# Kernel optimization log

Measured on AMD Instinct MI355X. Metric: run time of the kernel, lower is better.

Reference implementation:

```python
import jax, jax.numpy as jnp
import numpy as np
from jax import lax

B, T, D = 2, 2048, 2048
H, DK, DV = 16, 128, 128
K = 4  # conv kernel size
KEY_DIM = H * DK      # 2048
VAL_DIM = H * DV      # 2048
CONV_DIM = 2 * KEY_DIM + VAL_DIM  # 6144
EPS = 1e-6


def setup_inputs() -> dict:
    key = jax.random.key(0)
    ks = jax.random.split(key, 10)
    s = lambda fan: 1.0 / np.sqrt(fan)
    return {
        "hidden_states": jax.random.normal(ks[0], (B, T, D), jnp.float32),
        "W_qkv": jax.random.normal(ks[1], (D, CONV_DIM), jnp.float32) * s(D),
        "conv_w": jax.random.normal(ks[2], (CONV_DIM, 1, K), jnp.float32) * s(K),
        "W_z": jax.random.normal(ks[3], (D, VAL_DIM), jnp.float32) * s(D),
        "W_b": jax.random.normal(ks[4], (D, H), jnp.float32) * s(D),
        "W_a": jax.random.normal(ks[5], (D, H), jnp.float32) * s(D),
        "dt_bias": jnp.ones((H,), jnp.float32),
        "A_log": jnp.log(jax.random.uniform(ks[6], (H,), jnp.float32, 1e-3, 16.0)),
        "norm_weight": jnp.ones((DV,), jnp.float32),
        "W_out": jax.random.normal(ks[7], (VAL_DIM, D), jnp.float32) * s(VAL_DIM),
    }


def _l2norm(x):
    return x * lax.rsqrt(jnp.sum(x * x, axis=-1, keepdims=True) + 1e-6)


def _gated_delta_rule(q, k, v, g, beta):
    """q,k: [B,T,H,DK]; v: [B,T,H,DV]; g,beta: [B,T,H]. Returns o: [B,T,H,DV]."""
    # time-major for scan
    qT, kT, vT = (jnp.moveaxis(x, 1, 0) for x in (q, k, v))  # [T,B,H,d]
    gT = jnp.moveaxis(g, 1, 0)      # [T,B,H]
    bT = jnp.moveaxis(beta, 1, 0)   # [T,B,H]

    def step(S, inp):
        q_t, k_t, v_t, g_t, b_t = inp
        S = S * jnp.exp(g_t)[..., None, None]                      # decay [B,H,DK,DV]
        kv_mem = jnp.einsum("bhk,bhkv->bhv", k_t, S)               # S^T k
        delta = (v_t - kv_mem) * b_t[..., None]                     # beta-scaled error
        S = S + jnp.einsum("bhk,bhv->bhkv", k_t, delta)
        o_t = jnp.einsum("bhk,bhkv->bhv", q_t, S)
        return S, o_t

    S0 = jnp.zeros((q.shape[0], H, DK, DV), q.dtype)
    _, oT = lax.scan(step, S0, (qT, kT, vT, gT, bT))
    return jnp.moveaxis(oT, 0, 1)  # [B,T,H,DV]


def reference(hidden_states, W_qkv, conv_w, W_z, W_b, W_a, dt_bias, A_log,
              norm_weight, W_out):
    Bs, Ts, _ = hidden_states.shape

    # qkv projection + depthwise causal conv1d + silu
    mixed = hidden_states @ W_qkv                      # [B,T,CONV_DIM]
    xc = jnp.moveaxis(mixed, 1, 2)                     # [B,C,T]
    xc = lax.conv_general_dilated(xc, conv_w, (1,), [(K - 1, 0)],
                                  feature_group_count=CONV_DIM)
    mixed = jax.nn.silu(jnp.moveaxis(xc, 1, 2))        # [B,T,C]

    q, k, v = jnp.split(mixed, [KEY_DIM, 2 * KEY_DIM], axis=-1)
    q = _l2norm(q.reshape(Bs, Ts, H, DK)) * (DK ** -0.5)
    k = _l2norm(k.reshape(Bs, Ts, H, DK))
    v = v.reshape(Bs, Ts, H, DV)

    beta = jax.nn.sigmoid(hidden_states @ W_b)                     # [B,T,H]
    g = -jnp.exp(A_log) * jax.nn.softplus(hidden_states @ W_a + dt_bias)

    o = _gated_delta_rule(q, k, v, g, beta)            # [B,T,H,DV]

    # gated RMSNorm (Mamba2-style: gate first, then normalize)
    z = (hidden_states @ W_z).reshape(Bs, Ts, H, DV)
    o = o * jax.nn.silu(z)
    var = jnp.mean(o * o, axis=-1, keepdims=True)
    o = o * lax.rsqrt(var + EPS) * norm_weight

    return o.reshape(Bs, Ts, VAL_DIM) @ W_out          # [B,T,D]
```

## Files before the change

### kernel.cpp

```cpp
#include <hip/hip_runtime.h>

#define B_ 2
#define T_ 2048
#define D_ 2048
#define H_ 16
#define CONV_DIM_ 6144
#define NC_ 32
#define CK_ 64

typedef __bf16 bf16;
typedef bf16 bf16x8 __attribute__((ext_vector_type(8)));
typedef bf16 bf16x4 __attribute__((ext_vector_type(4)));
typedef float floatx4 __attribute__((ext_vector_type(4)));

__device__ __forceinline__ void async_copy16(bf16* lds, const bf16* g) {
    auto* g1 = (const __attribute__((address_space(1))) unsigned int*)g;
    auto* l3 = (__attribute__((address_space(3))) unsigned int*)lds;
    __builtin_amdgcn_global_load_lds(g1, l3, 16, 0, 0);
}

__global__ void cvt_bf16_kernel(const float* __restrict__ in, bf16* __restrict__ out, int n4) {
    int i = blockIdx.x * 256 + threadIdx.x;
    if (i < n4) {
        float4 v = ((const float4*)in)[i];
        bf16x4 o = { (bf16)v.x, (bf16)v.y, (bf16)v.z, (bf16)v.w };
        *(bf16x4*)(out + 4 * (size_t)i) = o;
    }
}

__global__ void transpose_kernel(const float* __restrict__ in, bf16* __restrict__ out, int R, int Cn) {
    __shared__ float tile[32][33];
    const int c0 = blockIdx.x << 5, r0 = blockIdx.y << 5;
    const int tx = threadIdx.x & 31, ty = threadIdx.x >> 5;
#pragma unroll
    for (int i = 0; i < 4; ++i) {
        int r = ty + (i << 3);
        tile[r][tx] = in[(size_t)(r0 + r) * Cn + c0 + tx];
    }
    __syncthreads();
#pragma unroll
    for (int i = 0; i < 4; ++i) {
        int cc = ty + (i << 3);
        out[(size_t)(c0 + cc) * R + r0 + tx] = (bf16)tile[tx][cc];
    }
}

__global__ void wba_cvt_kernel(const float* __restrict__ Wb, const float* __restrict__ Wa,
                               bf16* __restrict__ Wba) {
    int idx = blockIdx.x * 256 + threadIdx.x;
    int d = idx >> 4, h = idx & 15;
    Wba[(size_t)h * 2048 + d]        = (bf16)Wb[idx];
    Wba[(size_t)(h + 16) * 2048 + d] = (bf16)Wa[idx];
}

template <typename OutT>
__global__ __launch_bounds__(256) void gemm_kernel(
    const bf16* __restrict__ A, const bf16* __restrict__ Bt, OutT* __restrict__ C,
    int M, int N, int K) {
    __shared__ bf16 As[128 * 64];
    __shared__ bf16 Bs[128 * 64];
    const int tid = threadIdx.x;
    const int m0 = blockIdx.y << 7;
    const int n0 = blockIdx.x << 7;
    const int wave = tid >> 6, lane = tid & 63;
    const int wm = (wave >> 1) << 6, wn = (wave & 1) << 6;
    const int lrow = lane & 15, quad = lane >> 4;
    const int rl = lane >> 3;
    const int c8s = (lane & 7) ^ (rl & 7);

    floatx4 acc[4][4];
#pragma unroll
    for (int mt = 0; mt < 4; ++mt)
#pragma unroll
        for (int nt = 0; nt < 4; ++nt)
            acc[mt][nt] = floatx4{0.f, 0.f, 0.f, 0.f};

    for (int k0 = 0; k0 < K; k0 += 64) {
        __syncthreads();
#pragma unroll
        for (int i = 0; i < 4; ++i) {
            const int slot = wave * 4 + i;
            const int r = slot * 8 + rl;
            async_copy16(&As[slot * 512], A + (size_t)(m0 + r) * K + k0 + c8s * 8);
            async_copy16(&Bs[slot * 512], Bt + (size_t)(n0 + r) * K + k0 + c8s * 8);
        }
        __syncthreads();
#pragma unroll
        for (int kk = 0; kk < 64; kk += 32) {
            const int sw = (((kk >> 3) + quad) ^ (lrow & 7)) << 3;
            bf16x8 af[4], bfr[4];
#pragma unroll
            for (int mt = 0; mt < 4; ++mt) {
                af[mt]  = *(const bf16x8*)(&As[((wm + (mt << 4) + lrow) << 6) + sw]);
                bfr[mt] = *(const bf16x8*)(&Bs[((wn + (mt << 4) + lrow) << 6) + sw]);
            }
#pragma unroll
            for (int mt = 0; mt < 4; ++mt)
#pragma unroll
                for (int nt = 0; nt < 4; ++nt)
                    acc[mt][nt] = __builtin_amdgcn_mfma_f32_16x16x32_bf16(af[mt], bfr[nt], acc[mt][nt], 0, 0, 0);
        }
    }
#pragma unroll
    for (int mt = 0; mt < 4; ++mt)
#pragma unroll
        for (int nt = 0; nt < 4; ++nt) {
            const int col = n0 + wn + (nt << 4) + lrow;
            const int rowb = m0 + wm + (mt << 4) + (quad << 2);
#pragma unroll
            for (int i2 = 0; i2 < 4; ++i2)
                C[(size_t)(rowb + i2) * N + col] = (OutT)acc[mt][nt][i2];
        }
}

__global__ __launch_bounds__(512, 2) void gemm256_kernel(
    const bf16* __restrict__ A, const bf16* __restrict__ Bt,
    bf16* __restrict__ C0, bf16* __restrict__ C1,
    int M, int Ncat, int K, int split, int ld0, int ld1) {
    __shared__ bf16 As[4][256 * 32];
    __shared__ bf16 Bs[4][256 * 32];
    const int tid = threadIdx.x;
    const int wave = tid >> 6, lane = tid & 63;
    const int quad = lane >> 4, lrow = lane & 15;
    const int wm = (wave >> 2) << 7;
    const int wn = (wave & 3) << 6;
    const int m0 = blockIdx.y << 8, n0 = blockIdx.x << 8;

    const bf16* gA[2];
    const bf16* gB[2];
#pragma unroll
    for (int i = 0; i < 2; ++i) {
        const int q = wave * 2 + i;
        const int u = (lane & 7) ^ (lane >> 3);
        const int row = (q * 8 + (lane >> 3)) * 2 + (u >> 2);
        const int col = (u & 3) * 8;
        gA[i] = A  + (size_t)(m0 + row) * K + col;
        gB[i] = Bt + (size_t)(n0 + row) * K + col;
    }

    auto loff = [](int row, int qd) -> int {
        return ((row >> 1) << 6) + (((((row & 1) << 2) | qd) ^ ((row >> 1) & 7)) << 3);
    };

    floatx4 acc[8][4];
#pragma unroll
    for (int mt = 0; mt < 8; ++mt)
#pragma unroll
        for (int nt = 0; nt < 4; ++nt)
            acc[mt][nt] = floatx4{0.f, 0.f, 0.f, 0.f};

    const int KT = K >> 5;

#pragma unroll
    for (int t = 0; t < 3; ++t) {
        async_copy16(&As[t][(wave * 2 + 0) * 512], gA[0] + t * 32);
        async_copy16(&As[t][(wave * 2 + 1) * 512], gA[1] + t * 32);
        async_copy16(&Bs[t][(wave * 2 + 0) * 512], gB[0] + t * 32);
        async_copy16(&Bs[t][(wave * 2 + 1) * 512], gB[1] + t * 32);
    }
    asm volatile("s_waitcnt vmcnt(8)" ::: "memory");
    __builtin_amdgcn_s_barrier();

    for (int t = 0; t < KT; ++t) {
        const int b = t & 3;
        const bf16* as = &As[b][0];
        const bf16* bs = &Bs[b][0];
        bf16x8 bfr[4], af[4];
#pragma unroll
        for (int nt = 0; nt < 4; ++nt)
            bfr[nt] = *(const bf16x8*)(bs + loff(wn + nt * 16 + lrow, quad));
#pragma unroll
        for (int mt = 0; mt < 4; ++mt)
            af[mt] = *(const bf16x8*)(as + loff(wm + mt * 16 + lrow, quad));
        if (t + 2 < KT)       asm volatile("s_waitcnt vmcnt(4)" ::: "memory");
        else if (t + 2 == KT) asm volatile("s_waitcnt vmcnt(0)" ::: "memory");
        if (t + 3 < KT) {
            const int bn = (t + 3) & 3;
            async_copy16(&As[bn][(wave * 2 + 0) * 512], gA[0] + (t + 3) * 32);
            async_copy16(&As[bn][(wave * 2 + 1) * 512], gA[1] + (t + 3) * 32);
        }
        __builtin_amdgcn_s_barrier();
        asm volatile("s_waitcnt lgkmcnt(0)" ::: "memory");
        __builtin_amdgcn_sched_barrier(0);
        __builtin_amdgcn_s_setprio(1);
#pragma unroll
        for (int mt = 0; mt < 4; ++mt)
#pragma unroll
            for (int nt = 0; nt < 4; ++nt)
                acc[mt][nt] = __builtin_amdgcn_mfma_f32_16x16x32_bf16(
                    af[mt], bfr[nt], acc[mt][nt], 0, 0, 0);
        __builtin_amdgcn_s_setprio(0);
        __builtin_amdgcn_sched_barrier(0);
        __builtin_amdgcn_s_barrier();
#pragma unroll
        for (int mt = 0; mt < 4; ++mt)
            af[mt] = *(const bf16x8*)(as + loff(wm + 64 + mt * 16 + lrow, quad));
        if (t + 3 < KT) {
            const int bn = (t + 3) & 3;
            async_copy16(&Bs[bn][(wave * 2 + 0) * 512], gB[0] + (t + 3) * 32);
            async_copy16(&Bs[bn][(wave * 2 + 1) * 512], gB[1] + (t + 3) * 32);
        }
        __builtin_amdgcn_s_barrier();
        asm volatile("s_waitcnt lgkmcnt(0)" ::: "memory");
        __builtin_amdgcn_sched_barrier(0);
        __builtin_amdgcn_s_setprio(1);
#pragma unroll
        for (int mt = 0; mt < 4; ++mt)
#pragma unroll
            for (int nt = 0; nt < 4; ++nt)
                acc[4 + mt][nt] = __builtin_amdgcn_mfma_f32_16x16x32_bf16(
                    af[mt], bfr[nt], acc[4 + mt][nt], 0, 0, 0);
        __builtin_amdgcn_s_setprio(0);
        __builtin_amdgcn_sched_barrier(0);
        __builtin_amdgcn_s_barrier();
    }

    const bool second = (n0 >= split);
    bf16* Cp = second ? C1 : C0;
    const int ldc = second ? ld1 : ld0;
    const int nc0 = second ? n0 - split : n0;
#pragma unroll
    for (int mt = 0; mt < 8; ++mt)
#pragma unroll
        for (int nt = 0; nt < 4; ++nt) {
            const int col = nc0 + wn + nt * 16 + lrow;
            const int rowb = m0 + wm + mt * 16 + (quad << 2);
#pragma unroll
            for (int i2 = 0; i2 < 4; ++i2)
                Cp[(size_t)(rowb + i2) * ldc + col] = (bf16)acc[mt][nt][i2];
        }
}

__global__ __launch_bounds__(256) void conv_silu_kernel(
    const bf16* __restrict__ mixed, const float* __restrict__ cw,
    bf16* __restrict__ qb, bf16* __restrict__ kb, bf16* __restrict__ vb) {
    const int bt = blockIdx.y;
    const int t = bt & (T_ - 1);
    const int b = bt >> 11;
    const int c0 = blockIdx.x * 2048 + threadIdx.x * 8;
    const size_t base = (size_t)bt * CONV_DIM_ + c0;

    bf16x8 zz;
#pragma unroll
    for (int j = 0; j < 8; ++j) zz[j] = (bf16)0.f;
    const bf16x8 r3 = *(const bf16x8*)(mixed + base);
    const bf16x8 r2 = (t >= 1) ? *(const bf16x8*)(mixed + base - CONV_DIM_) : zz;
    const bf16x8 r1 = (t >= 2) ? *(const bf16x8*)(mixed + base - 2 * CONV_DIM_) : zz;
    const bf16x8 r0 = (t >= 3) ? *(const bf16x8*)(mixed + base - 3 * CONV_DIM_) : zz;

    const float4* cw4 = (const float4*)cw;
    float vals[8];
    float ss = 0.f;
#pragma unroll
    for (int j = 0; j < 8; ++j) {
        const float4 w = cw4[c0 + j];
        float acc = (float)r3[j] * w.w + (float)r2[j] * w.z +
                    (float)r1[j] * w.y + (float)r0[j] * w.x;
        const float sv = acc / (1.f + __expf(-acc));
        vals[j] = sv;
        ss += sv * sv;
    }

    if (c0 < 4096) {
#pragma unroll
        for (int o = 1; o < 16; o <<= 1) ss += __shfl_xor(ss, o);
        const float scale = rsqrtf(ss + 1e-6f);
        const bool isq = c0 < 2048;
        const float mul = isq ? scale * 0.08838834764831845f : scale;
        const int h = (c0 >> 7) & 15;
        const int d0 = c0 & 127;
        const size_t oidx = (((size_t)(b * H_ + h)) * T_ + t) * 128 + d0;
        bf16x8 o8;
#pragma unroll
        for (int j = 0; j < 8; ++j) o8[j] = (bf16)(vals[j] * mul);
        *(bf16x8*)((isq ? qb : kb) + oidx) = o8;
    } else {
        const int h = (c0 >> 7) & 15;
        const int d0 = c0 & 127;
        const size_t oidx = (((size_t)(b * H_ + h)) * T_ + t) * 128 + d0;
        bf16x8 o8;
#pragma unroll
        for (int j = 0; j < 8; ++j) o8[j] = (bf16)vals[j];
        *(bf16x8*)(vb + oidx) = o8;
    }
}

__global__ __launch_bounds__(256) void gbeta_mfma_kernel(
    const bf16* __restrict__ Xb, const bf16* __restrict__ Wba,
    const float* __restrict__ dtb, const float* __restrict__ Alog,
    float* __restrict__ gbuf, float* __restrict__ bbuf) {
    const int tid = threadIdx.x, wave = tid >> 6, lane = tid & 63;
    const int ln = lane & 15, qd = lane >> 4;
    const int m0 = blockIdx.x * 64 + wave * 16;
    floatx4 acc0 = {0.f, 0.f, 0.f, 0.f}, acc1 = {0.f, 0.f, 0.f, 0.f};
    const bf16* arow = Xb + (size_t)(m0 + ln) * 2048 + qd * 8;
    const bf16* b0 = Wba + (size_t)ln * 2048 + qd * 8;
    const bf16* b1 = Wba + (size_t)(16 + ln) * 2048 + qd * 8;
    for (int k = 0; k < 2048; k += 32) {
        bf16x8 af  = *(const bf16x8*)(arow + k);
        bf16x8 bf0 = *(const bf16x8*)(b0 + k);
        bf16x8 bf1 = *(const bf16x8*)(b1 + k);
        acc0 = __builtin_amdgcn_mfma_f32_16x16x32_bf16(af, bf0, acc0, 0, 0, 0);
        acc1 = __builtin_amdgcn_mfma_f32_16x16x32_bf16(af, bf1, acc1, 0, 0, 0);
    }
    const float dtbv = dtb[ln], al = __expf(Alog[ln]);
#pragma unroll
    for (int ii = 0; ii < 4; ++ii) {
        const int row = m0 + qd * 4 + ii;
        const int t = row & (T_ - 1), b = row >> 11;
        const size_t o = ((size_t)(b * H_ + ln)) * T_ + t;
        bbuf[o] = 1.f / (1.f + __expf(-acc0[ii]));
        const float xx = acc1[ii] + dtbv;
        const float sp = (xx > 15.f) ? xx : log1pf(__expf(xx));
        gbuf[o] = -al * sp;
    }
}

__global__ __launch_bounds__(256) void qkkt_kernel(const bf16* __restrict__ qb, const bf16* __restrict__ kb,
                                                   float* __restrict__ Araw, float* __restrict__ Mraw) {
    const int u = blockIdx.x;
    const int bh = u >> 5, nc = u & 31;
    const int t0 = nc * CK_;
    const int tid = threadIdx.x, wave = tid >> 6, lane = tid & 63;
    const int qd = lane >> 4, ln = lane & 15;
    __shared__ bf16 Kc[64 * 136], Qc[64 * 136];
    const size_t kbase = ((size_t)bh * T_ + t0) * 128;
#pragma unroll
    for (int it = 0; it < 4; ++it) {
        int idx = it * 256 + tid;
        int row = idx >> 4, c8 = idx & 15;
        *(uint4*)(&Kc[row * 136 + c8 * 8]) = *(const uint4*)(kb + kbase + row * 128 + c8 * 8);
        *(uint4*)(&Qc[row * 136 + c8 * 8]) = *(const uint4*)(qb + kbase + row * 128 + c8 * 8);
    }
    __syncthreads();
#pragma unroll
    for (int nt = 0; nt < 4; ++nt) {
        floatx4 accA = {0.f, 0.f, 0.f, 0.f}, accM = {0.f, 0.f, 0.f, 0.f};
#pragma unroll
        for (int kk = 0; kk < 4; ++kk) {
            bf16x8 bfr = *(const bf16x8*)(&Kc[(nt * 16 + ln) * 136 + kk * 32 + qd * 8]);
            bf16x8 afK = *(const bf16x8*)(&Kc[(wave * 16 + ln) * 136 + kk * 32 + qd * 8]);
            bf16x8 afQ = *(const bf16x8*)(&Qc[(wave * 16 + ln) * 136 + kk * 32 + qd * 8]);
            accA = __builtin_amdgcn_mfma_f32_16x16x32_bf16(afK, bfr, accA, 0, 0, 0);
            accM = __builtin_amdgcn_mfma_f32_16x16x32_bf16(afQ, bfr, accM, 0, 0, 0);
        }
#pragma unroll
        for (int ii = 0; ii < 4; ++ii) {
            int i = wave * 16 + qd * 4 + ii, j = nt * 16 + ln;
            Araw[(size_t)u * 4096 + i * 64 + j] = accA[ii];
            Mraw[(size_t)u * 4096 + i * 64 + j] = accM[ii];
        }
    }
}

__global__ __launch_bounds__(64) void prep_kernel(
    const float* __restrict__ gbuf, const float* __restrict__ bbuf,
    const float* __restrict__ Araw, const float* __restrict__ Mraw,
    float* __restrict__ lamg, float* __restrict__ ratiog,
    bf16* __restrict__ Tg, bf16* __restrict__ Mg) {
    const int u = blockIdx.x, bh = u >> 5, nc = u & 31, t0 = nc * CK_;
    const int lane = threadIdx.x;
    __shared__ float L[64 * 65];
    __shared__ float cv[64], bv[64];
    float g = gbuf[(size_t)bh * T_ + t0 + lane];
    float beta = bbuf[(size_t)bh * T_ + t0 + lane];
    float c = g;
#pragma unroll
    for (int off = 1; off < 64; off <<= 1) {
        float tval = __shfl_up(c, off);
        if (lane >= off) c += tval;
    }
    float c63 = __shfl(c, 63);
    lamg[(size_t)u * 64 + lane] = __expf(c);
    ratiog[(size_t)u * 64 + lane] = __expf(c63 - c);
    cv[lane] = c; bv[lane] = beta;
    __syncthreads();
    for (int i = 0; i < 64; ++i) {
        float a = Araw[(size_t)u * 4096 + i * 64 + lane];
        L[i * 65 + lane] = (lane < i) ? bv[i] * __expf(cv[i] - c) * a : 0.f;
    }
    __syncthreads();
    float t[64];
#pragma unroll
    for (int i = 0; i < 64; ++i) t[i] = (i == lane) ? 1.f : 0.f;
#pragma unroll
    for (int j = 0; j < 63; ++j) {
#pragma unroll
        for (int i = j + 1; i < 64; ++i)
            t[i] -= L[i * 65 + j] * t[j];
    }
#pragma unroll
    for (int i = 0; i < 64; ++i)
        Tg[(size_t)u * 4096 + i * 64 + lane] = (bf16)t[i];
    for (int i = 0; i < 64; ++i) {
        float m = Mraw[(size_t)u * 4096 + i * 64 + lane];
        float mij = (lane <= i) ? __expf(cv[i] - c) * m : 0.f;
        Mg[(size_t)u * 4096 + i * 64 + lane] = (bf16)mij;
    }
}

struct Pref {
    uint4 t2[2], m2[2];
    bf16x8 kf[4], qf[4];
    bf16x8 ktf[2][2];
    float rrv[4], vv[4], lam[4], bet[4], lamlast;
};

__device__ __forceinline__ void load_pref(
    Pref& p, int u, int t0, size_t kbase, int tid, int wave, int ln, int qd,
    int bh, int vbase,
    const bf16* __restrict__ qb, const bf16* __restrict__ kb, const bf16* __restrict__ vb,
    const bf16* __restrict__ Tg, const bf16* __restrict__ Mg,
    const float* __restrict__ lamg, const float* __restrict__ ratiog,
    const float* __restrict__ bbuf) {
#pragma unroll
    for (int it = 0; it < 2; ++it) {
        int idx = it * 256 + tid;
        int row = idx >> 3, c8 = idx & 7;
        p.t2[it] = *(const uint4*)(Tg + (size_t)u * 4096 + row * 64 + c8 * 8);
        p.m2[it] = *(const uint4*)(Mg + (size_t)u * 4096 + row * 64 + c8 * 8);
    }
    const size_t rowoff = kbase + (size_t)(wave * 16 + ln) * 128;
#pragma unroll
    for (int kk = 0; kk < 4; ++kk) {
        p.kf[kk] = *(const bf16x8*)(kb + rowoff + kk * 32 + qd * 8);
        p.qf[kk] = *(const bf16x8*)(qb + rowoff + kk * 32 + qd * 8);
    }
    const int i0 = wave * 16 + qd * 4;
#pragma unroll
    for (int ii = 0; ii < 4; ++ii) {
        p.vv[ii]  = (float)vb[kbase + (size_t)(i0 + ii) * 128 + vbase + ln];
        p.lam[ii] = lamg[(size_t)u * 64 + i0 + ii];
        p.bet[ii] = bbuf[(size_t)bh * T_ + t0 + i0 + ii];
        p.rrv[ii] = ratiog[(size_t)u * 64 + i0 + ii];
    }
    p.lamlast = lamg[(size_t)u * 64 + 63];
#pragma unroll
    for (int mt = 0; mt < 2; ++mt) {
        const int kd = (wave * 2 + mt) * 16 + ln;
#pragma unroll
        for (int kk2 = 0; kk2 < 2; ++kk2) {
            const int ib = kk2 * 32 + qd * 8;
#pragma unroll
            for (int j = 0; j < 8; ++j)
                p.ktf[mt][kk2][j] = kb[kbase + (size_t)(ib + j) * 128 + kd];
        }
    }
}

__global__ __launch_bounds__(256) void seq_kernel(
    const bf16* __restrict__ qb, const bf16* __restrict__ kb, const bf16* __restrict__ vb,
    const bf16* __restrict__ Tg, const bf16* __restrict__ Mg,
    const float* __restrict__ lamg, const float* __restrict__ ratiog,
    const float* __restrict__ bbuf, float* __restrict__ ob) {
    const int bh = blockIdx.x & 31;
    const int vs = blockIdx.x >> 5;
    const int vbase = vs * 16;
    const int tid = threadIdx.x;
    const int wave = tid >> 6, lane = tid & 63;
    const int qd = lane >> 4, ln = lane & 15;

    __shared__ bf16 Tt[64 * 72], Mm[64 * 72];
    __shared__ bf16 bT[16 * 72], Dt[16 * 72], Dtr[16 * 72];
    __shared__ bf16 Sbf[2][16 * 136];

    for (int idx = tid; idx < 2 * 16 * 136; idx += 256)
        (&Sbf[0][0])[idx] = (bf16)0.f;

    floatx4 Sreg[2] = { floatx4{0.f, 0.f, 0.f, 0.f}, floatx4{0.f, 0.f, 0.f, 0.f} };

    auto chunk_body = [&](Pref& cur, Pref& nxt, int nc, bf16* Srd, bf16* Swr) {
        const int t0 = nc * CK_;
        const size_t kbase = ((size_t)bh * T_ + t0) * 128;

#pragma unroll
        for (int it = 0; it < 2; ++it) {
            int idx = it * 256 + tid;
            int row = idx >> 3, c8 = idx & 7;
            *(uint4*)(&Tt[row * 72 + c8 * 8]) = cur.t2[it];
            *(uint4*)(&Mm[row * 72 + c8 * 8]) = cur.m2[it];
        }

        {
            const int ncn = (nc + 1 < NC_) ? nc + 1 : nc;
            load_pref(nxt, bh * NC_ + ncn, ncn * CK_, ((size_t)bh * T_ + (size_t)ncn * CK_) * 128,
                      tid, wave, ln, qd, bh, vbase, qb, kb, vb, Tg, Mg, lamg, ratiog, bbuf);
        }

        floatx4 ks = {0.f, 0.f, 0.f, 0.f};
#pragma unroll
        for (int kk = 0; kk < 4; ++kk) {
            bf16x8 bf = *(const bf16x8*)(&Srd[ln * 136 + kk * 32 + qd * 8]);
            ks = __builtin_amdgcn_mfma_f32_16x16x32_bf16(cur.kf[kk], bf, ks, 0, 0, 0);
        }
        {
            const int i0 = wave * 16 + qd * 4;
            bf16x4 bw;
#pragma unroll
            for (int ii = 0; ii < 4; ++ii)
                bw[ii] = (bf16)(cur.bet[ii] * (cur.vv[ii] - cur.lam[ii] * ks[ii]));
            *(bf16x4*)(&bT[ln * 72 + i0]) = bw;
        }
        __syncthreads();

        {
            floatx4 acc = {0.f, 0.f, 0.f, 0.f};
#pragma unroll
            for (int kk = 0; kk < 2; ++kk) {
                bf16x8 af = *(const bf16x8*)(&Tt[(wave * 16 + ln) * 72 + kk * 32 + qd * 8]);
                bf16x8 bf = *(const bf16x8*)(&bT[ln * 72 + kk * 32 + qd * 8]);
                acc = __builtin_amdgcn_mfma_f32_16x16x32_bf16(af, bf, acc, 0, 0, 0);
            }
            const int i0 = wave * 16 + qd * 4;
            bf16x4 dw = { (bf16)acc[0], (bf16)acc[1], (bf16)acc[2], (bf16)acc[3] };
            *(bf16x4*)(&Dt[ln * 72 + i0]) = dw;
            bf16x4 dwr = { (bf16)(acc[0] * cur.rrv[0]), (bf16)(acc[1] * cur.rrv[1]),
                           (bf16)(acc[2] * cur.rrv[2]), (bf16)(acc[3] * cur.rrv[3]) };
            *(bf16x4*)(&Dtr[ln * 72 + i0]) = dwr;
        }
        __syncthreads();

        {
            floatx4 acc = {0.f, 0.f, 0.f, 0.f};
#pragma unroll
            for (int kk = 0; kk < 4; ++kk) {
                bf16x8 bf = *(const bf16x8*)(&Srd[ln * 136 + kk * 32 + qd * 8]);
                acc = __builtin_amdgcn_mfma_f32_16x16x32_bf16(cur.qf[kk], bf, acc, 0, 0, 0);
            }
            floatx4 o;
#pragma unroll
            for (int ii = 0; ii < 4; ++ii) o[ii] = acc[ii] * cur.lam[ii];
#pragma unroll
            for (int kk = 0; kk < 2; ++kk) {
                bf16x8 af = *(const bf16x8*)(&Mm[(wave * 16 + ln) * 72 + kk * 32 + qd * 8]);
                bf16x8 bf = *(const bf16x8*)(&Dt[ln * 72 + kk * 32 + qd * 8]);
                o = __builtin_amdgcn_mfma_f32_16x16x32_bf16(af, bf, o, 0, 0, 0);
            }
            const int i0 = wave * 16 + qd * 4;
#pragma unroll
            for (int ii = 0; ii < 4; ++ii)
                ob[kbase + (size_t)(i0 + ii) * 128 + vbase + ln] = o[ii];
        }
#pragma unroll
        for (int mt = 0; mt < 2; ++mt) {
            const int kt = wave * 2 + mt;
            floatx4 acc = {0.f, 0.f, 0.f, 0.f};
#pragma unroll
            for (int kk = 0; kk < 2; ++kk) {
                bf16x8 bf = *(const bf16x8*)(&Dtr[ln * 72 + kk * 32 + qd * 8]);
                acc = __builtin_amdgcn_mfma_f32_16x16x32_bf16(cur.ktf[mt][kk], bf, acc, 0, 0, 0);
            }
            floatx4 sold = Sreg[mt];
#pragma unroll
            for (int ii = 0; ii < 4; ++ii) sold[ii] = sold[ii] * cur.lamlast + acc[ii];
            Sreg[mt] = sold;
            bf16x4 sb4 = { (bf16)sold[0], (bf16)sold[1], (bf16)sold[2], (bf16)sold[3] };
            *(bf16x4*)(&Swr[ln * 136 + kt * 16 + qd * 4]) = sb4;
        }
        __syncthreads();
    };

    Pref pA, pB;
    load_pref(pA, bh * NC_, 0, (size_t)bh * T_ * 128, tid, wave, ln, qd, bh, vbase,
              qb, kb, vb, Tg, Mg, lamg, ratiog, bbuf);
    __syncthreads();

#pragma unroll 1
    for (int nc2 = 0; nc2 < NC_; nc2 += 2) {
        chunk_body(pA, pB, nc2,     &Sbf[0][0], &Sbf[1][0]);
        chunk_body(pB, pA, nc2 + 1, &Sbf[1][0], &Sbf[0][0]);
    }
}

__global__ void gated_norm_kernel(const float* __restrict__ ob, const bf16* __restrict__ z,
                                  const float* __restrict__ nw, bf16* __restrict__ onorm) {
    const int idx = blockIdx.x;
    const int h = idx & (H_ - 1);
    const int bt = idx >> 4;
    const int t = bt & (T_ - 1);
    const int b = bt >> 11;
    const int tid = threadIdx.x;
    const size_t obase = (((size_t)(b * H_ + h)) * T_ + t) * 128;
    const size_t zbase = (size_t)bt * 2048 + (h << 7);
    float o1 = ob[obase + tid], o2 = ob[obase + tid + 64];
    const float z1 = (float)z[zbase + tid], z2 = (float)z[zbase + tid + 64];
    o1 *= z1 / (1.f + __expf(-z1));
    o2 *= z2 / (1.f + __expf(-z2));
    float ss = o1 * o1 + o2 * o2;
#pragma unroll
    for (int o = 1; o < 64; o <<= 1) ss += __shfl_xor(ss, o);
    const float scale = rsqrtf(ss * (1.f / 128.f) + 1e-6f);
    onorm[zbase + tid]      = (bf16)(o1 * scale * nw[tid]);
    onorm[zbase + tid + 64] = (bf16)(o2 * scale * nw[tid + 64]);
}

extern "C" void kernel_launch(void* const* d_in, const int* in_sizes, int n_in,
                              void* d_out, int out_size, void* d_ws, size_t ws_size,
                              hipStream_t stream) {
    const float* X    = (const float*)d_in[0];
    const float* Wqkv = (const float*)d_in[1];
    const float* cw   = (const float*)d_in[2];
    const float* Wz   = (const float*)d_in[3];
    const float* Wb   = (const float*)d_in[4];
    const float* Wa   = (const float*)d_in[5];
    const float* dtb  = (const float*)d_in[6];
    const float* Alog = (const float*)d_in[7];
    const float* nw   = (const float*)d_in[8];
    const float* Wout = (const float*)d_in[9];
    float* out = (float*)d_out;

    char* ws = (char*)d_ws;
    size_t off = 0;
    auto alloc = [&](size_t bytes) -> char* {
        char* p = ws + off;
        off += (bytes + 255) & ~(size_t)255;
        return p;
    };
    bf16*  Xb      = (bf16*)alloc((size_t)B_ * T_ * D_ * 2);
    char*  wcat_p  = alloc((size_t)8192 * 2048 * 2);
    bf16*  Wcat    = (bf16*)wcat_p;
    bf16*  Woutt   = (bf16*)alloc((size_t)D_ * D_ * 2);
    bf16*  Wba     = (bf16*)alloc((size_t)32 * 2048 * 2);
    char*  mixed_p = alloc((size_t)B_ * T_ * CONV_DIM_ * 2);
    bf16*  mixedb  = (bf16*)mixed_p;
    bf16*  zb      = (bf16*)alloc((size_t)B_ * T_ * D_ * 2);
    bf16*  kbuf    = (bf16*)alloc((size_t)B_ * T_ * D_ * 2);
    bf16*  vbuf    = (bf16*)alloc((size_t)B_ * T_ * D_ * 2);
    float* gbuf    = (float*)alloc((size_t)B_ * T_ * H_ * 4);
    float* bbuf    = (float*)alloc((size_t)B_ * T_ * H_ * 4);
    float* Mraw    = (float*)alloc((size_t)1024 * 4096 * 4);
    bf16*  Tg      = (bf16*)alloc((size_t)1024 * 4096 * 2);
    bf16*  Mg      = (bf16*)alloc((size_t)1024 * 4096 * 2);
    float* lamg    = (float*)alloc((size_t)1024 * 64 * 4);
    float* ratiog  = (float*)alloc((size_t)1024 * 64 * 4);
    bf16*  qbuf    = (bf16*)wcat_p;
    float* obuf    = (float*)mixed_p;
    float* Araw    = (float*)(mixed_p + (size_t)B_ * T_ * D_ * 4);
    bf16*  onorm   = (bf16*)Xb;

    cvt_bf16_kernel<<<dim3((B_ * T_ * D_ / 4 + 255) / 256), dim3(256), 0, stream>>>(X, Xb, B_ * T_ * D_ / 4);
    transpose_kernel<<<dim3(CONV_DIM_ / 32, D_ / 32), dim3(256), 0, stream>>>(Wqkv, Wcat, D_, CONV_DIM_);
    transpose_kernel<<<dim3(D_ / 32, D_ / 32), dim3(256), 0, stream>>>(Wz, Wcat + (size_t)CONV_DIM_ * D_, D_, D_);
    transpose_kernel<<<dim3(D_ / 32, D_ / 32), dim3(256), 0, stream>>>(Wout, Woutt, D_, D_);
    wba_cvt_kernel<<<dim3(128), dim3(256), 0, stream>>>(Wb, Wa, Wba);

    gemm256_kernel<<<dim3(8192 / 256, B_ * T_ / 256), dim3(512), 0, stream>>>(
        Xb, Wcat, mixedb, zb, B_ * T_, 8192, D_, CONV_DIM_, CONV_DIM_, D_);

    gbeta_mfma_kernel<<<dim3(64), dim3(256), 0, stream>>>(Xb, Wba, dtb, Alog, gbuf, bbuf);
    conv_silu_kernel<<<dim3(CONV_DIM_ / 2048, B_ * T_), dim3(256), 0, stream>>>(mixedb, cw, qbuf, kbuf, vbuf);

    qkkt_kernel<<<dim3(1024), dim3(256), 0, stream>>>(qbuf, kbuf, Araw, Mraw);
    prep_kernel<<<dim3(1024), dim3(64), 0, stream>>>(gbuf, bbuf, Araw, Mraw, lamg, ratiog, Tg, Mg);
    seq_kernel<<<dim3(256), dim3(256), 0, stream>>>(qbuf, kbuf, vbuf, Tg, Mg, lamg, ratiog, bbuf, obuf);

    gated_norm_kernel<<<dim3(B_ * T_ * H_), dim3(64), 0, stream>>>(obuf, zb, nw, onorm);

    gemm_kernel<float><<<dim3(D_ / 128, B_ * T_ / 128), dim3(256), 0, stream>>>(
        onorm, Woutt, out, B_ * T_, D_, D_);
}
```

Measured before the change: 602.4 us.

## Fuse QK^T and chunk prep kernels, split sequential scan into narrower value slices

Merges qkkt_kernel and prep_kernel into one kernel. The Gram matrices now stay in LDS instead of making an fp32 round trip through global memory. Inside that kernel, wave 0 runs the triangular solve while the other waves build the masked decay matrix. The sequential scan now covers 8 value columns per block instead of 16, doubling the grid to 512 blocks for more parallelism. In exchange, half of every MFMA tile in the scan is padding, so the compute per block stays the same while the total MFMA work doubles.

```diff
diff --git a/kernel.cpp b/kernel.cpp
--- a/kernel.cpp
+++ b/kernel.cpp
@@ -316,14 +316,19 @@
     }
 }
 
-__global__ __launch_bounds__(256) void qkkt_kernel(const bf16* __restrict__ qb, const bf16* __restrict__ kb,
-                                                   float* __restrict__ Araw, float* __restrict__ Mraw) {
+__global__ __launch_bounds__(256) void qkkt_prep_kernel(
+    const bf16* __restrict__ qb, const bf16* __restrict__ kb,
+    const float* __restrict__ gbuf, const float* __restrict__ bbuf,
+    float* __restrict__ lamg, float* __restrict__ ratiog,
+    bf16* __restrict__ Tg, bf16* __restrict__ Mg) {
     const int u = blockIdx.x;
     const int bh = u >> 5, nc = u & 31;
     const int t0 = nc * CK_;
     const int tid = threadIdx.x, wave = tid >> 6, lane = tid & 63;
     const int qd = lane >> 4, ln = lane & 15;
     __shared__ bf16 Kc[64 * 136], Qc[64 * 136];
+    __shared__ float Af[64 * 65], Mf[64 * 65];
+    __shared__ float cv[64], bv[64];
     const size_t kbase = ((size_t)bh * T_ + t0) * 128;
 #pragma unroll
     for (int it = 0; it < 4; ++it) {
@@ -332,7 +337,22 @@
         *(uint4*)(&Kc[row * 136 + c8 * 8]) = *(const uint4*)(kb + kbase + row * 128 + c8 * 8);
         *(uint4*)(&Qc[row * 136 + c8 * 8]) = *(const uint4*)(qb + kbase + row * 128 + c8 * 8);
     }
+    if (wave == 0) {
+        float g = gbuf[(size_t)bh * T_ + t0 + lane];
+        float beta = bbuf[(size_t)bh * T_ + t0 + lane];
+        float c = g;
+#pragma unroll
+        for (int off = 1; off < 64; off <<= 1) {
+            float tval = __shfl_up(c, off);
+            if (lane >= off) c += tval;
+        }
+        float c63 = __shfl(c, 63);
+        lamg[(size_t)u * 64 + lane] = __expf(c);
+        ratiog[(size_t)u * 64 + lane] = __expf(c63 - c);
+        cv[lane] = c; bv[lane] = beta;
+    }
     __syncthreads();
+    floatx4 rA[4], rM[4];
 #pragma unroll
     for (int nt = 0; nt < 4; ++nt) {
         floatx4 accA = {0.f, 0.f, 0.f, 0.f}, accM = {0.f, 0.f, 0.f, 0.f};
@@ -344,58 +364,43 @@
             accA = __builtin_amdgcn_mfma_f32_16x16x32_bf16(afK, bfr, accA, 0, 0, 0);
             accM = __builtin_amdgcn_mfma_f32_16x16x32_bf16(afQ, bfr, accM, 0, 0, 0);
         }
+        rA[nt] = accA; rM[nt] = accM;
+    }
+#pragma unroll
+    for (int nt = 0; nt < 4; ++nt)
 #pragma unroll
         for (int ii = 0; ii < 4; ++ii) {
             int i = wave * 16 + qd * 4 + ii, j = nt * 16 + ln;
-            Araw[(size_t)u * 4096 + i * 64 + j] = accA[ii];
-            Mraw[(size_t)u * 4096 + i * 64 + j] = accM[ii];
-        }
-    }
-}
-
-__global__ __launch_bounds__(64) void prep_kernel(
-    const float* __restrict__ gbuf, const float* __restrict__ bbuf,
-    const float* __restrict__ Araw, const float* __restrict__ Mraw,
-    float* __restrict__ lamg, float* __restrict__ ratiog,
-    bf16* __restrict__ Tg, bf16* __restrict__ Mg) {
-    const int u = blockIdx.x, bh = u >> 5, nc = u & 31, t0 = nc * CK_;
-    const int lane = threadIdx.x;
-    __shared__ float L[64 * 65];
-    __shared__ float cv[64], bv[64];
-    float g = gbuf[(size_t)bh * T_ + t0 + lane];
-    float beta = bbuf[(size_t)bh * T_ + t0 + lane];
-    float c = g;
-#pragma unroll
-    for (int off = 1; off < 64; off <<= 1) {
-        float tval = __shfl_up(c, off);
-        if (lane >= off) c += tval;
-    }
-    float c63 = __shfl(c, 63);
-    lamg[(size_t)u * 64 + lane] = __expf(c);
-    ratiog[(size_t)u * 64 + lane] = __expf(c63 - c);
-    cv[lane] = c; bv[lane] = beta;
+            Af[i * 65 + j] = rA[nt][ii];
+            Mf[i * 65 + j] = rM[nt][ii];
+        }
     __syncthreads();
-    for (int i = 0; i < 64; ++i) {
-        float a = Araw[(size_t)u * 4096 + i * 64 + lane];
-        L[i * 65 + lane] = (lane < i) ? bv[i] * __expf(cv[i] - c) * a : 0.f;
+#pragma unroll
+    for (int r = 0; r < 16; ++r) {
+        const int i = wave * 16 + r;
+        float a = Af[i * 65 + lane];
+        Af[i * 65 + lane] = (lane < i) ? bv[i] * __expf(cv[i] - cv[lane]) * a : 0.f;
     }
     __syncthreads();
-    float t[64];
-#pragma unroll
-    for (int i = 0; i < 64; ++i) t[i] = (i == lane) ? 1.f : 0.f;
-#pragma unroll
-    for (int j = 0; j < 63; ++j) {
-#pragma unroll
-        for (int i = j + 1; i < 64; ++i)
-            t[i] -= L[i * 65 + j] * t[j];
-    }
-#pragma unroll
-    for (int i = 0; i < 64; ++i)
-        Tg[(size_t)u * 4096 + i * 64 + lane] = (bf16)t[i];
-    for (int i = 0; i < 64; ++i) {
-        float m = Mraw[(size_t)u * 4096 + i * 64 + lane];
-        float mij = (lane <= i) ? __expf(cv[i] - c) * m : 0.f;
-        Mg[(size_t)u * 4096 + i * 64 + lane] = (bf16)mij;
+    if (wave == 0) {
+        float t[64];
+#pragma unroll
+        for (int i = 0; i < 64; ++i) t[i] = (i == lane) ? 1.f : 0.f;
+#pragma unroll
+        for (int j = 0; j < 63; ++j) {
+#pragma unroll
+            for (int i = j + 1; i < 64; ++i)
+                t[i] -= Af[i * 65 + j] * t[j];
+        }
+#pragma unroll
+        for (int i = 0; i < 64; ++i)
+            Tg[(size_t)u * 4096 + i * 64 + lane] = (bf16)t[i];
+    } else {
+        for (int i = wave - 1; i < 64; i += 3) {
+            float m = Mf[i * 65 + lane];
+            float mij = (lane <= i) ? __expf(cv[i] - cv[lane]) * m : 0.f;
+            Mg[(size_t)u * 4096 + i * 64 + lane] = (bf16)mij;
+        }
     }
 }
 
@@ -429,7 +434,7 @@
     const int i0 = wave * 16 + qd * 4;
 #pragma unroll
     for (int ii = 0; ii < 4; ++ii) {
-        p.vv[ii]  = (float)vb[kbase + (size_t)(i0 + ii) * 128 + vbase + ln];
+        p.vv[ii]  = (ln < 8) ? (float)vb[kbase + (size_t)(i0 + ii) * 128 + vbase + ln] : 0.f;
         p.lam[ii] = lamg[(size_t)u * 64 + i0 + ii];
         p.bet[ii] = bbuf[(size_t)bh * T_ + t0 + i0 + ii];
         p.rrv[ii] = ratiog[(size_t)u * 64 + i0 + ii];
@@ -455,7 +460,7 @@
     const float* __restrict__ bbuf, float* __restrict__ ob) {
     const int bh = blockIdx.x & 31;
     const int vs = blockIdx.x >> 5;
-    const int vbase = vs * 16;
+    const int vbase = vs * 8;
     const int tid = threadIdx.x;
     const int wave = tid >> 6, lane = tid & 63;
     const int qd = lane >> 4, ln = lane & 15;
@@ -466,6 +471,9 @@
 
     for (int idx = tid; idx < 2 * 16 * 136; idx += 256)
         (&Sbf[0][0])[idx] = (bf16)0.f;
+    for (int idx = tid; idx < 16 * 72; idx += 256) {
+        bT[idx] = (bf16)0.f; Dt[idx] = (bf16)0.f; Dtr[idx] = (bf16)0.f;
+    }
 
     floatx4 Sreg[2] = { floatx4{0.f, 0.f, 0.f, 0.f}, floatx4{0.f, 0.f, 0.f, 0.f} };
 
@@ -537,9 +545,11 @@
                 o = __builtin_amdgcn_mfma_f32_16x16x32_bf16(af, bf, o, 0, 0, 0);
             }
             const int i0 = wave * 16 + qd * 4;
-#pragma unroll
-            for (int ii = 0; ii < 4; ++ii)
-                ob[kbase + (size_t)(i0 + ii) * 128 + vbase + ln] = o[ii];
+            if (ln < 8) {
+#pragma unroll
+                for (int ii = 0; ii < 4; ++ii)
+                    ob[kbase + (size_t)(i0 + ii) * 128 + vbase + ln] = o[ii];
+            }
         }
 #pragma unroll
         for (int mt = 0; mt < 2; ++mt) {
@@ -628,14 +638,12 @@
     bf16*  vbuf    = (bf16*)alloc((size_t)B_ * T_ * D_ * 2);
     float* gbuf    = (float*)alloc((size_t)B_ * T_ * H_ * 4);
     float* bbuf    = (float*)alloc((size_t)B_ * T_ * H_ * 4);
-    float* Mraw    = (float*)alloc((size_t)1024 * 4096 * 4);
     bf16*  Tg      = (bf16*)alloc((size_t)1024 * 4096 * 2);
     bf16*  Mg      = (bf16*)alloc((size_t)1024 * 4096 * 2);
     float* lamg    = (float*)alloc((size_t)1024 * 64 * 4);
     float* ratiog  = (float*)alloc((size_t)1024 * 64 * 4);
     bf16*  qbuf    = (bf16*)wcat_p;
     float* obuf    = (float*)mixed_p;
-    float* Araw    = (float*)(mixed_p + (size_t)B_ * T_ * D_ * 4);
     bf16*  onorm   = (bf16*)Xb;
 
     cvt_bf16_kernel<<<dim3((B_ * T_ * D_ / 4 + 255) / 256), dim3(256), 0, stream>>>(X, Xb, B_ * T_ * D_ / 4);
@@ -650,9 +658,8 @@
     gbeta_mfma_kernel<<<dim3(64), dim3(256), 0, stream>>>(Xb, Wba, dtb, Alog, gbuf, bbuf);
     conv_silu_kernel<<<dim3(CONV_DIM_ / 2048, B_ * T_), dim3(256), 0, stream>>>(mixedb, cw, qbuf, kbuf, vbuf);
 
-    qkkt_kernel<<<dim3(1024), dim3(256), 0, stream>>>(qbuf, kbuf, Araw, Mraw);
-    prep_kernel<<<dim3(1024), dim3(64), 0, stream>>>(gbuf, bbuf, Araw, Mraw, lamg, ratiog, Tg, Mg);
-    seq_kernel<<<dim3(256), dim3(256), 0, stream>>>(qbuf, kbuf, vbuf, Tg, Mg, lamg, ratiog, bbuf, obuf);
+    qkkt_prep_kernel<<<dim3(1024), dim3(256), 0, stream>>>(qbuf, kbuf, gbuf, bbuf, lamg, ratiog, Tg, Mg);
+    seq_kernel<<<dim3(512), dim3(256), 0, stream>>>(qbuf, kbuf, vbuf, Tg, Mg, lamg, ratiog, bbuf, obuf);
 
     gated_norm_kernel<<<dim3(B_ * T_ * H_), dim3(64), 0, stream>>>(obuf, zb, nw, onorm);
 
```

New measurement: 703.4 us. 16.8% more time.
